# Performance work log

Measured on AMD Instinct MI355X. Metric: run time of the kernel, lower is better.

The kernel has to match this reference:

```python
import jax, jax.numpy as jnp
import numpy as np


def setup_inputs() -> dict:
    key = jax.random.key(0)
    k1, k2, k3 = jax.random.split(key, 3)
    dim = 192
    x = jax.random.normal(k1, (4, dim, 256, 256), dtype=jnp.float32)
    # Conv2d(5*dim, dim, 1): weight [dim, 5*dim], bias [dim]
    W = jax.random.normal(k2, (dim, 5 * dim), dtype=jnp.float32) * 0.02
    b = jax.random.normal(k3, (dim,), dtype=jnp.float32) * 0.02
    return {"x": x, "W": W, "b": b}


def _shifts(x):
    # Matches torch: cat([x,
    #   pad(x[:,:,:,1:], (0,1)),   # take right neighbor (zero at last col)
    #   pad(x[:,:,:,:-1], (1,0)),  # take left neighbor (zero at first col)
    #   pad(x[:,:,1:,:], (0,0,0,1)),  # take below neighbor (zero at last row)
    #   pad(x[:,:,:-1,:], (0,0,1,0))  # take above neighbor (zero at first row)
    # ], dim=1)
    right = jnp.pad(x[:, :, :, 1:], ((0, 0), (0, 0), (0, 0), (0, 1)))
    left = jnp.pad(x[:, :, :, :-1], ((0, 0), (0, 0), (0, 0), (1, 0)))
    down = jnp.pad(x[:, :, 1:, :], ((0, 0), (0, 0), (0, 1), (0, 0)))
    up = jnp.pad(x[:, :, :-1, :], ((0, 0), (0, 0), (1, 0), (0, 0)))
    return jnp.concatenate([x, right, left, down, up], axis=1)  # [B, 5C, H, W]


def reference(x, W, b):
    xs = _shifts(x)  # [B, 5C, H, W]
    # 1x1 conv == per-pixel matmul over channels
    out = jnp.einsum("bchw,oc->bohw", xs, W) + b[None, :, None, None]
    return out
```

## Files before the change

kernel.cpp:

```cpp
#include <hip/hip_runtime.h>
#include <hip/hip_bf16.h>
#include <stdint.h>

#define CDIM 192
#define KDIM 960
#define HW   65536
#define WI   256

#define OFF_BIAS 368640u
#define NEED_WS  369408u

#define ROW_B    80
#define SLICE_B  10560
#define LDS_TOT  31680

typedef __attribute__((ext_vector_type(8))) short short8;
typedef __attribute__((ext_vector_type(4))) float floatx4;

__device__ __forceinline__ uint16_t f2b(float v) {
    __hip_bfloat16 h = __float2bfloat16(v);
    return *reinterpret_cast<uint16_t*>(&h);
}

__device__ __forceinline__ int detect_f(const void* xsrc) {
    const uint32_t* xw = (const uint32_t*)xsrc;
    uint32_t d = xw[(size_t)threadIdx.x * 98083u];
    uint32_t e = (d >> 7) & 0xFF;
    int isb = (e >= 110 && e <= 130) ? 1 : 0;
    return (__syncthreads_count(isb) >= 128) ? 1 : 0;
}

__global__ __launch_bounds__(256) void prep_kernel(const void* __restrict__ Wsrc,
                                                   const void* __restrict__ bsrc,
                                                   const void* __restrict__ xsrc,
                                                   __hip_bfloat16* __restrict__ Wb,
                                                   float* __restrict__ bfp) {
    const int f = detect_f(xsrc);
    if (blockIdx.x < 720) {
        int i = blockIdx.x * 256 + threadIdx.x;
        float v = f ? __bfloat162float(((const __hip_bfloat16*)Wsrc)[i])
                    : ((const float*)Wsrc)[i];
        Wb[i] = __float2bfloat16(v);
    } else if (threadIdx.x < CDIM) {
        int j = threadIdx.x;
        bfp[j] = f ? __bfloat162float(((const __hip_bfloat16*)bsrc)[j])
                   : ((const float*)bsrc)[j];
    }
}

__global__ __launch_bounds__(256, 3) void fused_kernel(const void* __restrict__ xsrc,
                                                       const __hip_bfloat16* __restrict__ Wm,
                                                       const float* __restrict__ biasf,
                                                       void* __restrict__ outv) {
    __shared__ char xsl[LDS_TOT];
    const int tid  = threadIdx.x;
    const int lane = tid & 63, wave = tid >> 6;
    const int quad = lane >> 4, l15 = lane & 15;

    const int f = detect_f(xsrc);

    const int nwg  = (int)gridDim.x;
    const int bid0 = (int)blockIdx.x;
    const int wg   = (bid0 & 7) * (nwg >> 3) + (bid0 >> 3);

    const int bb = wg >> 9;
    const int r  = wg & 511;
    const int h  = r >> 1;
    const int w0 = (r & 1) << 7;
    const int p0 = h * WI + w0;
    const int obase = (wave >> 1) * 96;
    const int nbase = (wave & 1) * 64;

    const char* wbase[6];
    #pragma unroll
    for (int mt = 0; mt < 6; ++mt) {
        int o = obase + mt * 16 + l15;
        wbase[mt] = (const char*)Wm + (size_t)o * (KDIM * 2) + quad * 16;
    }

    int pxa[4]; bool w255[4], wzero[4];
    #pragma unroll
    for (int nt = 0; nt < 4; ++nt) {
        int pl = nbase + nt * 16 + l15;
        pxa[nt]   = (pl + 1) * ROW_B;
        w255[nt]  = ((w0 + pl) == 255);
        wzero[nt] = ((w0 + pl) == 0);
    }

    const int scc  = tid >> 7;
    const int spx  = (tid & 127) + 1;
    const int scol = w0 + (tid & 127);
    const int ec = tid >> 1, ee = tid & 1;
    int ecol = ee ? (w0 + 128) : (w0 - 1);
    if (ecol < 0) ecol = 0;
    if (ecol > 255) ecol = 255;
    const int epx = ee ? 129 : 0;

    const size_t esz = f ? 2u : 4u;
    const char* xp = (const char*)xsrc + (size_t)bb * CDIM * HW * esz;

    int hr[3];
    #pragma unroll
    for (int rr = 0; rr < 3; ++rr) {
        int v = h - 1 + rr;
        hr[rr] = v < 0 ? 0 : (v > 255 ? 255 : v);
    }

    floatx4 acc[6][4];
    #pragma unroll
    for (int mt = 0; mt < 6; ++mt)
        #pragma unroll
        for (int nt = 0; nt < 4; ++nt)
            acc[mt][nt] = (floatx4){0.f, 0.f, 0.f, 0.f};

#define STAGE(JJ)                                                                          \
    {                                                                                      \
        const int c0 = (JJ) * 32;                                                          \
        _Pragma("unroll")                                                                  \
        for (int rr = 0; rr < 3; ++rr) {                                                   \
            uint32_t tmp[16];                                                              \
            const size_t rowoff = (size_t)hr[rr] * WI;                                     \
            if (f) {                                                                       \
                const uint16_t* xg = (const uint16_t*)xp;                                  \
                _Pragma("unroll")                                                          \
                for (int cc = 0; cc < 16; ++cc)                                            \
                    tmp[cc] = xg[(size_t)(c0 + scc * 16 + cc) * HW + rowoff + scol];       \
            } else {                                                                       \
                const float* xg = (const float*)xp;                                        \
                _Pragma("unroll")                                                          \
                for (int cc = 0; cc < 16; ++cc)                                            \
                    tmp[cc] = f2b(xg[(size_t)(c0 + scc * 16 + cc) * HW + rowoff + scol]);  \
            }                                                                              \
            uint4 q0, q1;                                                                  \
            q0.x = tmp[0] | (tmp[1] << 16);  q0.y = tmp[2] | (tmp[3] << 16);               \
            q0.z = tmp[4] | (tmp[5] << 16);  q0.w = tmp[6] | (tmp[7] << 16);               \
            q1.x = tmp[8] | (tmp[9] << 16);  q1.y = tmp[10] | (tmp[11] << 16);             \
            q1.z = tmp[12] | (tmp[13] << 16); q1.w = tmp[14] | (tmp[15] << 16);            \
            char* base = xsl + rr * SLICE_B + spx * ROW_B + scc * 32;                      \
            *(uint4*)(base)      = q0;                                                     \
            *(uint4*)(base + 16) = q1;                                                     \
        }                                                                                  \
        if (tid < 64) {                                                                    \
            _Pragma("unroll")                                                              \
            for (int rr = 0; rr < 3; ++rr) {                                               \
                const size_t gi = (size_t)(c0 + ec) * HW + (size_t)hr[rr] * WI + ecol;     \
                uint16_t v = f ? ((const uint16_t*)xp)[gi]                                 \
                               : f2b(((const float*)xp)[gi]);                              \
                *(uint16_t*)(xsl + rr * SLICE_B + epx * ROW_B + ec * 2) = v;               \
            }                                                                              \
        }                                                                                  \
    }

    STAGE(0)
    __syncthreads();

    for (int j = 0; j < 6; ++j) {
        #pragma unroll
        for (int s = 0; s < 5; ++s) {
            const int step = s * 6 + j;

            short8 af[6];
            #pragma unroll
            for (int mt = 0; mt < 6; ++mt)
                af[mt] = *(const short8*)(wbase[mt] + (size_t)step * 64);

            const int so   = (s == 3) ? 2 * SLICE_B : (s == 4) ? 0 : SLICE_B;
            const int dw80 = (s == 1) ? ROW_B : (s == 2) ? -ROW_B : 0;
            const bool skip = (s == 3 && h == 255) || (s == 4 && h == 0);
            short8 bf[4];
            #pragma unroll
            for (int nt = 0; nt < 4; ++nt) {
                short8 v = *(const short8*)(xsl + so + pxa[nt] + dw80 + quad * 16);
                const bool kill = skip || (s == 1 && w255[nt]) || (s == 2 && wzero[nt]);
                bf[nt] = kill ? (short8){0, 0, 0, 0, 0, 0, 0, 0} : v;
            }

            __builtin_amdgcn_s_setprio(1);
            #pragma unroll
            for (int mt = 0; mt < 6; ++mt)
                #pragma unroll
                for (int nt = 0; nt < 4; ++nt)
                    acc[mt][nt] = __builtin_amdgcn_mfma_f32_16x16x32_bf16(
                        af[mt], bf[nt], acc[mt][nt], 0, 0, 0);
            __builtin_amdgcn_s_setprio(0);
        }
        if (j < 5) {
            __syncthreads();
            STAGE(j + 1)
            __syncthreads();
        }
    }

    #pragma unroll
    for (int mt = 0; mt < 6; ++mt) {
        int o0 = obase + mt * 16 + quad * 4;
        float bv[4];
        #pragma unroll
        for (int rr = 0; rr < 4; ++rr) bv[rr] = biasf[o0 + rr];
        #pragma unroll
        for (int nt = 0; nt < 4; ++nt) {
            int px = nbase + nt * 16 + l15;
            size_t base = ((size_t)(bb * CDIM + o0) * HW) + p0 + px;
            if (f) {
                __hip_bfloat16* out = (__hip_bfloat16*)outv;
                #pragma unroll
                for (int rr = 0; rr < 4; ++rr)
                    out[base + (size_t)rr * HW] = __float2bfloat16(acc[mt][nt][rr] + bv[rr]);
            } else {
                float* out = (float*)outv;
                #pragma unroll
                for (int rr = 0; rr < 4; ++rr)
                    out[base + (size_t)rr * HW] = acc[mt][nt][rr] + bv[rr];
            }
        }
    }
#undef STAGE
}

__global__ __launch_bounds__(256) void fallback_kernel(const void* __restrict__ xv,
                                                       const void* __restrict__ Wv,
                                                       const void* __restrict__ bv,
                                                       void* __restrict__ outv) {
    __shared__ float Wl[KDIM];
    const int f = detect_f(xv);
    const int tid = threadIdx.x;
    const int bid = blockIdx.x;
    const int h = bid & 255;
    const int bo = bid >> 8;
    const int o = bo % CDIM;
    const int b = bo / CDIM;
    if (f) {
        const __hip_bfloat16* W16 = (const __hip_bfloat16*)Wv;
        for (int i = tid; i < KDIM; i += 256) Wl[i] = __bfloat162float(W16[(size_t)o * KDIM + i]);
    } else {
        const float* W32 = (const float*)Wv;
        for (int i = tid; i < KDIM; i += 256) Wl[i] = W32[(size_t)o * KDIM + i];
    }
    __syncthreads();
    const size_t pb = (size_t)b * CDIM * HW + (size_t)h * WI + tid;
    float acc = f ? __bfloat162float(((const __hip_bfloat16*)bv)[o]) : ((const float*)bv)[o];
    if (f) {
        const __hip_bfloat16* x = (const __hip_bfloat16*)xv;
        for (int c = 0; c < CDIM; ++c) {
            const __hip_bfloat16* xp = x + pb + (size_t)c * HW;
            float ctr = __bfloat162float(xp[0]);
            float rgt = (tid < 255) ? __bfloat162float(xp[1])   : 0.f;
            float lft = (tid > 0)   ? __bfloat162float(xp[-1])  : 0.f;
            float dwn = (h < 255)   ? __bfloat162float(xp[WI])  : 0.f;
            float up  = (h > 0)     ? __bfloat162float(xp[-WI]) : 0.f;
            acc += ctr * Wl[c] + rgt * Wl[192 + c] + lft * Wl[384 + c]
                 + dwn * Wl[576 + c] + up * Wl[768 + c];
        }
    } else {
        const float* x = (const float*)xv;
        for (int c = 0; c < CDIM; ++c) {
            const float* xp = x + pb + (size_t)c * HW;
            float ctr = xp[0];
            float rgt = (tid < 255) ? xp[1]   : 0.f;
            float lft = (tid > 0)   ? xp[-1]  : 0.f;
            float dwn = (h < 255)   ? xp[WI]  : 0.f;
            float up  = (h > 0)     ? xp[-WI] : 0.f;
            acc += ctr * Wl[c] + rgt * Wl[192 + c] + lft * Wl[384 + c]
                 + dwn * Wl[576 + c] + up * Wl[768 + c];
        }
    }
    size_t oidx = (size_t)bo * HW + (size_t)h * WI + tid;
    if (f) ((__hip_bfloat16*)outv)[oidx] = __float2bfloat16(acc);
    else   ((float*)outv)[oidx] = acc;
}

extern "C" void kernel_launch(void* const* d_in, const int* in_sizes, int n_in,
                              void* d_out, int out_size, void* d_ws, size_t ws_size,
                              hipStream_t stream) {
    (void)in_sizes; (void)n_in; (void)out_size;
    char* ws = (char*)d_ws;

    if (ws_size >= NEED_WS) {
        __hip_bfloat16* Wb = (__hip_bfloat16*)ws;
        float* bfp = (float*)(ws + OFF_BIAS);
        prep_kernel<<<721, 256, 0, stream>>>(d_in[1], d_in[2], d_in[0], Wb, bfp);
        fused_kernel<<<2048, 256, 0, stream>>>(d_in[0], Wb, bfp, d_out);
    } else {
        fallback_kernel<<<4 * CDIM * 256, 256, 0, stream>>>(d_in[0], d_in[1], d_in[2], d_out);
    }
}
```

Baseline: 535.4 us.

## Double-buffer LDS activation tiles and prefetch next chunk into registers during MFMA

The LDS staging buffer for the shifted activation rows is doubled so the next 32-channel chunk can be written while the current one is being read. Global loads for the next chunk are issued into registers partway through the current chunk's MFMA loop, then written to the alternate buffer afterwards. This removes one barrier per iteration and hides global load latency behind compute. In exchange it uses twice the LDS and about 51 extra staging registers per thread, and lowers the occupancy target from 3 to 2 workgroups per CU.

```diff
diff --git a/kernel.cpp b/kernel.cpp
--- a/kernel.cpp
+++ b/kernel.cpp
@@ -12,7 +12,8 @@
 
 #define ROW_B    80
 #define SLICE_B  10560
-#define LDS_TOT  31680
+#define HALF_B   31680
+#define LDS_TOT  63360
 
 typedef __attribute__((ext_vector_type(8))) short short8;
 typedef __attribute__((ext_vector_type(4))) float floatx4;
@@ -48,7 +49,7 @@
     }
 }
 
-__global__ __launch_bounds__(256, 3) void fused_kernel(const void* __restrict__ xsrc,
+__global__ __launch_bounds__(256, 2) void fused_kernel(const void* __restrict__ xsrc,
                                                        const __hip_bfloat16* __restrict__ Wm,
                                                        const float* __restrict__ biasf,
                                                        void* __restrict__ outv) {
@@ -113,48 +114,72 @@
         for (int nt = 0; nt < 4; ++nt)
             acc[mt][nt] = (floatx4){0.f, 0.f, 0.f, 0.f};
 
-#define STAGE(JJ)                                                                          \
+    uint32_t stg[3][16];
+    uint32_t stge[3];
+
+#define STAGE_LOAD(JJ)                                                                     \
     {                                                                                      \
         const int c0 = (JJ) * 32;                                                          \
         _Pragma("unroll")                                                                  \
         for (int rr = 0; rr < 3; ++rr) {                                                   \
-            uint32_t tmp[16];                                                              \
             const size_t rowoff = (size_t)hr[rr] * WI;                                     \
             if (f) {                                                                       \
                 const uint16_t* xg = (const uint16_t*)xp;                                  \
                 _Pragma("unroll")                                                          \
                 for (int cc = 0; cc < 16; ++cc)                                            \
-                    tmp[cc] = xg[(size_t)(c0 + scc * 16 + cc) * HW + rowoff + scol];       \
+                    stg[rr][cc] = xg[(size_t)(c0 + scc * 16 + cc) * HW + rowoff + scol];   \
             } else {                                                                       \
                 const float* xg = (const float*)xp;                                        \
                 _Pragma("unroll")                                                          \
                 for (int cc = 0; cc < 16; ++cc)                                            \
-                    tmp[cc] = f2b(xg[(size_t)(c0 + scc * 16 + cc) * HW + rowoff + scol]);  \
+                    stg[rr][cc] = __float_as_uint(                                         \
+                        xg[(size_t)(c0 + scc * 16 + cc) * HW + rowoff + scol]);            \
             }                                                                              \
+        }                                                                                  \
+        if (tid < 64) {                                                                    \
+            _Pragma("unroll")                                                              \
+            for (int rr = 0; rr < 3; ++rr) {                                               \
+                const size_t gi = (size_t)(c0 + ec) * HW + (size_t)hr[rr] * WI + ecol;     \
+                stge[rr] = f ? (uint32_t)((const uint16_t*)xp)[gi]                         \
+                             : __float_as_uint(((const float*)xp)[gi]);                    \
+            }                                                                              \
+        }                                                                                  \
+    }
+
+#define STAGE_WRITE(BOFF)                                                                  \
+    {                                                                                      \
+        _Pragma("unroll")                                                                  \
+        for (int rr = 0; rr < 3; ++rr) {                                                   \
+            uint32_t w_[16];                                                               \
+            _Pragma("unroll")                                                              \
+            for (int cc = 0; cc < 16; ++cc)                                                \
+                w_[cc] = f ? stg[rr][cc]                                                   \
+                           : (uint32_t)f2b(__uint_as_float(stg[rr][cc]));                  \
             uint4 q0, q1;                                                                  \
-            q0.x = tmp[0] | (tmp[1] << 16);  q0.y = tmp[2] | (tmp[3] << 16);               \
-            q0.z = tmp[4] | (tmp[5] << 16);  q0.w = tmp[6] | (tmp[7] << 16);               \
-            q1.x = tmp[8] | (tmp[9] << 16);  q1.y = tmp[10] | (tmp[11] << 16);             \
-            q1.z = tmp[12] | (tmp[13] << 16); q1.w = tmp[14] | (tmp[15] << 16);            \
-            char* base = xsl + rr * SLICE_B + spx * ROW_B + scc * 32;                      \
+            q0.x = w_[0] | (w_[1] << 16);   q0.y = w_[2] | (w_[3] << 16);                  \
+            q0.z = w_[4] | (w_[5] << 16);   q0.w = w_[6] | (w_[7] << 16);                  \
+            q1.x = w_[8] | (w_[9] << 16);   q1.y = w_[10] | (w_[11] << 16);                \
+            q1.z = w_[12] | (w_[13] << 16); q1.w = w_[14] | (w_[15] << 16);                \
+            char* base = xsl + (BOFF) + rr * SLICE_B + spx * ROW_B + scc * 32;             \
             *(uint4*)(base)      = q0;                                                     \
             *(uint4*)(base + 16) = q1;                                                     \
         }                                                                                  \
         if (tid < 64) {                                                                    \
             _Pragma("unroll")                                                              \
             for (int rr = 0; rr < 3; ++rr) {                                               \
-                const size_t gi = (size_t)(c0 + ec) * HW + (size_t)hr[rr] * WI + ecol;     \
-                uint16_t v = f ? ((const uint16_t*)xp)[gi]                                 \
-                               : f2b(((const float*)xp)[gi]);                              \
-                *(uint16_t*)(xsl + rr * SLICE_B + epx * ROW_B + ec * 2) = v;               \
+                uint16_t v = f ? (uint16_t)stge[rr]                                        \
+                               : f2b(__uint_as_float(stge[rr]));                           \
+                *(uint16_t*)(xsl + (BOFF) + rr * SLICE_B + epx * ROW_B + ec * 2) = v;      \
             }                                                                              \
         }                                                                                  \
     }
 
-    STAGE(0)
+    STAGE_LOAD(0)
+    STAGE_WRITE(0)
     __syncthreads();
 
     for (int j = 0; j < 6; ++j) {
+        const int cb = (j & 1) * HALF_B;
         #pragma unroll
         for (int s = 0; s < 5; ++s) {
             const int step = s * 6 + j;
@@ -170,7 +195,7 @@
             short8 bf[4];
             #pragma unroll
             for (int nt = 0; nt < 4; ++nt) {
-                short8 v = *(const short8*)(xsl + so + pxa[nt] + dw80 + quad * 16);
+                short8 v = *(const short8*)(xsl + cb + so + pxa[nt] + dw80 + quad * 16);
                 const bool kill = skip || (s == 1 && w255[nt]) || (s == 2 && wzero[nt]);
                 bf[nt] = kill ? (short8){0, 0, 0, 0, 0, 0, 0, 0} : v;
             }
@@ -183,10 +208,14 @@
                     acc[mt][nt] = __builtin_amdgcn_mfma_f32_16x16x32_bf16(
                         af[mt], bf[nt], acc[mt][nt], 0, 0, 0);
             __builtin_amdgcn_s_setprio(0);
+
+            if (s == 1 && j < 5) {
+                STAGE_LOAD(j + 1)
+                __builtin_amdgcn_sched_barrier(0);
+            }
         }
         if (j < 5) {
-            __syncthreads();
-            STAGE(j + 1)
+            STAGE_WRITE(((j + 1) & 1) * HALF_B)
             __syncthreads();
         }
     }
@@ -214,7 +243,8 @@
             }
         }
     }
-#undef STAGE
+#undef STAGE_LOAD
+#undef STAGE_WRITE
 }
 
 __global__ __launch_bounds__(256) void fallback_kernel(const void* __restrict__ xv,
```

After: 515.3 us. 3.8% less time.

## Double-buffer weight tiles in LDS via async global_load_lds with 512-thread blocks

Applied to the files above, without the earlier changes.

The fused kernel moves to 512 threads per block, with each wave owning 3 instead of 6 output-channel tiles. Weight fragments are now streamed into a double-buffered LDS area using asynchronous global-to-LDS loads, instead of every wave reading them straight from global memory. Staging of the shifted input slices is spread over the larger block. The aim is to cut redundant global weight traffic and raise occupancy and latency hiding, at the cost of extra barriers for each k-step and more LDS per block.

```diff
diff --git a/kernel.cpp b/kernel.cpp
--- a/kernel.cpp
+++ b/kernel.cpp
@@ -12,7 +12,8 @@
 
 #define ROW_B    80
 #define SLICE_B  10560
-#define LDS_TOT  31680
+#define LDS_X    31680
+#define WBUF     12288
 
 typedef __attribute__((ext_vector_type(8))) short short8;
 typedef __attribute__((ext_vector_type(4))) float floatx4;
@@ -22,12 +23,12 @@
     return *reinterpret_cast<uint16_t*>(&h);
 }
 
-__device__ __forceinline__ int detect_f(const void* xsrc) {
+__device__ __forceinline__ int detect_f(const void* xsrc, int nthr, uint32_t stride) {
     const uint32_t* xw = (const uint32_t*)xsrc;
-    uint32_t d = xw[(size_t)threadIdx.x * 98083u];
+    uint32_t d = xw[(size_t)threadIdx.x * stride];
     uint32_t e = (d >> 7) & 0xFF;
     int isb = (e >= 110 && e <= 130) ? 1 : 0;
-    return (__syncthreads_count(isb) >= 128) ? 1 : 0;
+    return (__syncthreads_count(isb) >= (nthr >> 1)) ? 1 : 0;
 }
 
 __global__ __launch_bounds__(256) void prep_kernel(const void* __restrict__ Wsrc,
@@ -35,7 +36,7 @@
                                                    const void* __restrict__ xsrc,
                                                    __hip_bfloat16* __restrict__ Wb,
                                                    float* __restrict__ bfp) {
-    const int f = detect_f(xsrc);
+    const int f = detect_f(xsrc, 256, 98083u);
     if (blockIdx.x < 720) {
         int i = blockIdx.x * 256 + threadIdx.x;
         float v = f ? __bfloat162float(((const __hip_bfloat16*)Wsrc)[i])
@@ -48,16 +49,17 @@
     }
 }
 
-__global__ __launch_bounds__(256, 3) void fused_kernel(const void* __restrict__ xsrc,
+__global__ __launch_bounds__(512, 4) void fused_kernel(const void* __restrict__ xsrc,
                                                        const __hip_bfloat16* __restrict__ Wm,
                                                        const float* __restrict__ biasf,
                                                        void* __restrict__ outv) {
-    __shared__ char xsl[LDS_TOT];
+    __shared__ char xsl[LDS_X];
+    __shared__ char ldsW[2 * WBUF];
     const int tid  = threadIdx.x;
     const int lane = tid & 63, wave = tid >> 6;
     const int quad = lane >> 4, l15 = lane & 15;
 
-    const int f = detect_f(xsrc);
+    const int f = detect_f(xsrc, 512, 49109u);
 
     const int nwg  = (int)gridDim.x;
     const int bid0 = (int)blockIdx.x;
@@ -68,14 +70,22 @@
     const int h  = r >> 1;
     const int w0 = (r & 1) << 7;
     const int p0 = h * WI + w0;
-    const int obase = (wave >> 1) * 96;
+    const int obase = (wave >> 1) * 48;
     const int nbase = (wave & 1) * 64;
 
-    const char* wbase[6];
-    #pragma unroll
-    for (int mt = 0; mt < 6; ++mt) {
+    const int ch0 = tid;
+    const char* gw0 = (const char*)Wm + ((size_t)(ch0 % 192) * KDIM + (ch0 / 192) * 8) * 2;
+    const int lo0 = ch0 * 16;
+    const int ch1 = tid + 512;
+    const char* gw1 = (const char*)Wm + ((size_t)(ch1 % 192) * KDIM + (ch1 / 192) * 8) * 2;
+    const int lo1 = ch1 * 16;
+    const bool wlow = (wave < 4);
+
+    int aoff[3];
+    #pragma unroll
+    for (int mt = 0; mt < 3; ++mt) {
         int o = obase + mt * 16 + l15;
-        wbase[mt] = (const char*)Wm + (size_t)o * (KDIM * 2) + quad * 16;
+        aoff[mt] = (quad * 192 + o) * 16;
     }
 
     int pxa[4]; bool w255[4], wzero[4];
@@ -87,10 +97,11 @@
         wzero[nt] = ((w0 + pl) == 0);
     }
 
-    const int scc  = tid >> 7;
+    const int scc  = (tid >> 7) & 3;
     const int spx  = (tid & 127) + 1;
     const int scol = w0 + (tid & 127);
-    const int ec = tid >> 1, ee = tid & 1;
+    const int erow = tid >> 6;
+    const int ec = (tid & 63) >> 1, ee = tid & 1;
     int ecol = ee ? (w0 + 128) : (w0 - 1);
     if (ecol < 0) ecol = 0;
     if (ecol > 255) ecol = 255;
@@ -105,10 +116,11 @@
         int v = h - 1 + rr;
         hr[rr] = v < 0 ? 0 : (v > 255 ? 255 : v);
     }
-
-    floatx4 acc[6][4];
-    #pragma unroll
-    for (int mt = 0; mt < 6; ++mt)
+    const int ehr = (erow == 0) ? hr[0] : (erow == 1 ? hr[1] : hr[2]);
+
+    floatx4 acc[3][4];
+    #pragma unroll
+    for (int mt = 0; mt < 3; ++mt)
         #pragma unroll
         for (int nt = 0; nt < 4; ++nt)
             acc[mt][nt] = (floatx4){0.f, 0.f, 0.f, 0.f};
@@ -118,51 +130,77 @@
         const int c0 = (JJ) * 32;                                                          \
         _Pragma("unroll")                                                                  \
         for (int rr = 0; rr < 3; ++rr) {                                                   \
-            uint32_t tmp[16];                                                              \
+            uint32_t tmp[8];                                                               \
             const size_t rowoff = (size_t)hr[rr] * WI;                                     \
             if (f) {                                                                       \
                 const uint16_t* xg = (const uint16_t*)xp;                                  \
                 _Pragma("unroll")                                                          \
-                for (int cc = 0; cc < 16; ++cc)                                            \
-                    tmp[cc] = xg[(size_t)(c0 + scc * 16 + cc) * HW + rowoff + scol];       \
+                for (int cc = 0; cc < 8; ++cc)                                             \
+                    tmp[cc] = xg[(size_t)(c0 + scc * 8 + cc) * HW + rowoff + scol];        \
             } else {                                                                       \
                 const float* xg = (const float*)xp;                                        \
                 _Pragma("unroll")                                                          \
-                for (int cc = 0; cc < 16; ++cc)                                            \
-                    tmp[cc] = f2b(xg[(size_t)(c0 + scc * 16 + cc) * HW + rowoff + scol]);  \
+                for (int cc = 0; cc < 8; ++cc)                                             \
+                    tmp[cc] = f2b(xg[(size_t)(c0 + scc * 8 + cc) * HW + rowoff + scol]);   \
             }                                                                              \
-            uint4 q0, q1;                                                                  \
-            q0.x = tmp[0] | (tmp[1] << 16);  q0.y = tmp[2] | (tmp[3] << 16);               \
-            q0.z = tmp[4] | (tmp[5] << 16);  q0.w = tmp[6] | (tmp[7] << 16);               \
-            q1.x = tmp[8] | (tmp[9] << 16);  q1.y = tmp[10] | (tmp[11] << 16);             \
-            q1.z = tmp[12] | (tmp[13] << 16); q1.w = tmp[14] | (tmp[15] << 16);            \
-            char* base = xsl + rr * SLICE_B + spx * ROW_B + scc * 32;                      \
-            *(uint4*)(base)      = q0;                                                     \
-            *(uint4*)(base + 16) = q1;                                                     \
+            uint4 q;                                                                       \
+            q.x = tmp[0] | (tmp[1] << 16);  q.y = tmp[2] | (tmp[3] << 16);                 \
+            q.z = tmp[4] | (tmp[5] << 16);  q.w = tmp[6] | (tmp[7] << 16);                 \
+            *(uint4*)(xsl + rr * SLICE_B + spx * ROW_B + scc * 16) = q;                    \
         }                                                                                  \
-        if (tid < 64) {                                                                    \
-            _Pragma("unroll")                                                              \
-            for (int rr = 0; rr < 3; ++rr) {                                               \
-                const size_t gi = (size_t)(c0 + ec) * HW + (size_t)hr[rr] * WI + ecol;     \
-                uint16_t v = f ? ((const uint16_t*)xp)[gi]                                 \
-                               : f2b(((const float*)xp)[gi]);                              \
-                *(uint16_t*)(xsl + rr * SLICE_B + epx * ROW_B + ec * 2) = v;               \
-            }                                                                              \
+        if (tid < 192) {                                                                   \
+            const size_t gi = (size_t)(c0 + ec) * HW + (size_t)ehr * WI + ecol;            \
+            uint16_t v = f ? ((const uint16_t*)xp)[gi]                                     \
+                           : f2b(((const float*)xp)[gi]);                                  \
+            *(uint16_t*)(xsl + erow * SLICE_B + epx * ROW_B + ec * 2) = v;                 \
         }                                                                                  \
     }
 
+    gload16_helper:;
+    {
+        __builtin_amdgcn_global_load_lds(
+            (const __attribute__((address_space(1))) uint32_t*)gw0,
+            (__attribute__((address_space(3))) uint32_t*)(ldsW + lo0), 16, 0, 0);
+        if (wlow)
+            __builtin_amdgcn_global_load_lds(
+                (const __attribute__((address_space(1))) uint32_t*)gw1,
+                (__attribute__((address_space(3))) uint32_t*)(ldsW + lo1), 16, 0, 0);
+    }
     STAGE(0)
     __syncthreads();
 
     for (int j = 0; j < 6; ++j) {
         #pragma unroll
         for (int s = 0; s < 5; ++s) {
-            const int step = s * 6 + j;
-
-            short8 af[6];
+            const int cur = (s & 1) * WBUF;
+            __builtin_amdgcn_s_barrier();
+            __builtin_amdgcn_sched_barrier(0);
+            if (s < 4) {
+                const int nxt = WBUF - cur;
+                const size_t woff = (size_t)((s + 1) * 6 + j) * 64;
+                __builtin_amdgcn_global_load_lds(
+                    (const __attribute__((address_space(1))) uint32_t*)(gw0 + woff),
+                    (__attribute__((address_space(3))) uint32_t*)(ldsW + nxt + lo0), 16, 0, 0);
+                if (wlow)
+                    __builtin_amdgcn_global_load_lds(
+                        (const __attribute__((address_space(1))) uint32_t*)(gw1 + woff),
+                        (__attribute__((address_space(3))) uint32_t*)(ldsW + nxt + lo1), 16, 0, 0);
+            }
+            __builtin_amdgcn_sched_barrier(0);
+            if (s < 4) {
+                if (wlow) asm volatile("s_waitcnt vmcnt(2)" ::: "memory");
+                else      asm volatile("s_waitcnt vmcnt(1)" ::: "memory");
+            } else {
+                asm volatile("s_waitcnt vmcnt(0)" ::: "memory");
+            }
+            __builtin_amdgcn_sched_barrier(0);
+            __builtin_amdgcn_s_barrier();
+            __builtin_amdgcn_sched_barrier(0);
+
+            short8 af[3];
             #pragma unroll
-            for (int mt = 0; mt < 6; ++mt)
-                af[mt] = *(const short8*)(wbase[mt] + (size_t)step * 64);
+            for (int mt = 0; mt < 3; ++mt)
+                af[mt] = *(const short8*)(ldsW + cur + aoff[mt]);
 
             const int so   = (s == 3) ? 2 * SLICE_B : (s == 4) ? 0 : SLICE_B;
             const int dw80 = (s == 1) ? ROW_B : (s == 2) ? -ROW_B : 0;
@@ -177,7 +215,7 @@
 
             __builtin_amdgcn_s_setprio(1);
             #pragma unroll
-            for (int mt = 0; mt < 6; ++mt)
+            for (int mt = 0; mt < 3; ++mt)
                 #pragma unroll
                 for (int nt = 0; nt < 4; ++nt)
                     acc[mt][nt] = __builtin_amdgcn_mfma_f32_16x16x32_bf16(
@@ -186,13 +224,23 @@
         }
         if (j < 5) {
             __syncthreads();
+            {
+                const size_t woff = (size_t)(j + 1) * 64;
+                __builtin_amdgcn_global_load_lds(
+                    (const __attribute__((address_space(1))) uint32_t*)(gw0 + woff),
+                    (__attribute__((address_space(3))) uint32_t*)(ldsW + lo0), 16, 0, 0);
+                if (wlow)
+                    __builtin_amdgcn_global_load_lds(
+                        (const __attribute__((address_space(1))) uint32_t*)(gw1 + woff),
+                        (__attribute__((address_space(3))) uint32_t*)(ldsW + lo1), 16, 0, 0);
+            }
             STAGE(j + 1)
             __syncthreads();
         }
     }
 
     #pragma unroll
-    for (int mt = 0; mt < 6; ++mt) {
+    for (int mt = 0; mt < 3; ++mt) {
         int o0 = obase + mt * 16 + quad * 4;
         float bv[4];
         #pragma unroll
@@ -222,7 +270,7 @@
                                                        const void* __restrict__ bv,
                                                        void* __restrict__ outv) {
     __shared__ float Wl[KDIM];
-    const int f = detect_f(xv);
+    const int f = detect_f(xv, 256, 98083u);
     const int tid = threadIdx.x;
     const int bid = blockIdx.x;
     const int h = bid & 255;
@@ -279,7 +327,7 @@
         __hip_bfloat16* Wb = (__hip_bfloat16*)ws;
         float* bfp = (float*)(ws + OFF_BIAS);
         prep_kernel<<<721, 256, 0, stream>>>(d_in[1], d_in[2], d_in[0], Wb, bfp);
-        fused_kernel<<<2048, 256, 0, stream>>>(d_in[0], Wb, bfp, d_out);
+        fused_kernel<<<2048, 512, 0, stream>>>(d_in[0], Wb, bfp, d_out);
     } else {
         fallback_kernel<<<4 * CDIM * 256, 256, 0, stream>>>(d_in[0], d_in[1], d_in[2], d_out);
     }
```

Measured after the change: 486.6 us. -9.1%, faster.

## Stage weight tiles into double-buffered LDS with async global_load_lds

Applied to the files above, without the earlier changes.

Each wave used to read its weight fragments straight from global memory. Now a double-buffered 2x12KB LDS weight area is filled with global_load_lds, prefetching the next K-step's weights while the current step's MFMAs run, and fragments are read from LDS. This cuts redundant global/L2 weight traffic across waves. In exchange it adds two block barriers per K-step and larger LDS use, and lowers launch bounds occupancy from 3 to 2 workgroups per CU.

```diff
diff --git a/kernel.cpp b/kernel.cpp
--- a/kernel.cpp
+++ b/kernel.cpp
@@ -12,7 +12,8 @@
 
 #define ROW_B    80
 #define SLICE_B  10560
-#define LDS_TOT  31680
+#define WOFF     31680
+#define WBUF     12288
 
 typedef __attribute__((ext_vector_type(8))) short short8;
 typedef __attribute__((ext_vector_type(4))) float floatx4;
@@ -48,11 +49,19 @@
     }
 }
 
-__global__ __launch_bounds__(256, 3) void fused_kernel(const void* __restrict__ xsrc,
+__device__ __forceinline__ void gload16(const void* g, void* l) {
+    __builtin_amdgcn_global_load_lds(
+        (const __attribute__((address_space(1))) uint32_t*)g,
+        (__attribute__((address_space(3))) uint32_t*)l, 16, 0, 0);
+}
+
+__global__ __launch_bounds__(256, 2) void fused_kernel(const void* __restrict__ xsrc,
                                                        const __hip_bfloat16* __restrict__ Wm,
                                                        const float* __restrict__ biasf,
                                                        void* __restrict__ outv) {
-    __shared__ char xsl[LDS_TOT];
+    __shared__ char lds[WOFF + 2 * WBUF];
+    char* xsl  = lds;
+    char* ldsW = lds + WOFF;
     const int tid  = threadIdx.x;
     const int lane = tid & 63, wave = tid >> 6;
     const int quad = lane >> 4, l15 = lane & 15;
@@ -71,11 +80,20 @@
     const int obase = (wave >> 1) * 96;
     const int nbase = (wave & 1) * 64;
 
-    const char* wbase[6];
+    const char* gw[3];
+    int ldsoff[3];
+    #pragma unroll
+    for (int t = 0; t < 3; ++t) {
+        int chunk = tid + t * 256;
+        int kq = chunk / 192, o = chunk % 192;
+        gw[t] = (const char*)Wm + ((size_t)o * KDIM + kq * 8) * 2;
+        ldsoff[t] = chunk * 16;
+    }
+    int aoff[6];
     #pragma unroll
     for (int mt = 0; mt < 6; ++mt) {
         int o = obase + mt * 16 + l15;
-        wbase[mt] = (const char*)Wm + (size_t)o * (KDIM * 2) + quad * 16;
+        aoff[mt] = (quad * 192 + o) * 16;
     }
 
     int pxa[4]; bool w255[4], wzero[4];
@@ -151,18 +169,34 @@
         }                                                                                  \
     }
 
+    #pragma unroll
+    for (int t = 0; t < 3; ++t) gload16(gw[t], ldsW + ldsoff[t]);
     STAGE(0)
     __syncthreads();
 
     for (int j = 0; j < 6; ++j) {
         #pragma unroll
         for (int s = 0; s < 5; ++s) {
-            const int step = s * 6 + j;
+            const int cur = (s & 1) * WBUF;
+            __builtin_amdgcn_s_barrier();
+            __builtin_amdgcn_sched_barrier(0);
+            if (s < 4) {
+                const int nxt = WBUF - cur;
+                #pragma unroll
+                for (int t = 0; t < 3; ++t)
+                    gload16(gw[t] + (size_t)((s + 1) * 6 + j) * 64, ldsW + nxt + ldsoff[t]);
+            }
+            __builtin_amdgcn_sched_barrier(0);
+            if (s < 4) asm volatile("s_waitcnt vmcnt(3)" ::: "memory");
+            else       asm volatile("s_waitcnt vmcnt(0)" ::: "memory");
+            __builtin_amdgcn_sched_barrier(0);
+            __builtin_amdgcn_s_barrier();
+            __builtin_amdgcn_sched_barrier(0);
 
             short8 af[6];
             #pragma unroll
             for (int mt = 0; mt < 6; ++mt)
-                af[mt] = *(const short8*)(wbase[mt] + (size_t)step * 64);
+                af[mt] = *(const short8*)(ldsW + cur + aoff[mt]);
 
             const int so   = (s == 3) ? 2 * SLICE_B : (s == 4) ? 0 : SLICE_B;
             const int dw80 = (s == 1) ? ROW_B : (s == 2) ? -ROW_B : 0;
@@ -186,6 +220,9 @@
         }
         if (j < 5) {
             __syncthreads();
+            #pragma unroll
+            for (int t = 0; t < 3; ++t)
+                gload16(gw[t] + (size_t)(j + 1) * 64, ldsW + ldsoff[t]);
             STAGE(j + 1)
             __syncthreads();
         }
```

Result: faster. 468.0 us (-12.6%).
